# Optimization experiments

Measured on AMD Instinct MI355X. Metric: run time of the kernel, lower is better.

## Reference

```python
import jax, jax.numpy as jnp
import numpy as np

G = 4          # deformable groups (from offset_and_mask_dim = 3*4*3*3)
K = 9          # 3x3 kernel points
GN_GROUPS = 16 # GroupNorm groups as in DyHead


def conv2d(x, w, stride=1, pad=1, groups=1):
    return jax.lax.conv_general_dilated(
        x, w, (stride, stride), [(pad, pad), (pad, pad)],
        dimension_numbers=('NCHW', 'OIHW', 'NCHW'),
        feature_group_count=groups)


def dw_conv(x, w, scale, bias):
    # YOLO Conv with g=in_channels: depthwise 3x3 + folded BN + SiLU
    C = x.shape[1]
    y = conv2d(x, w, groups=C)
    y = y * scale[None, :, None, None] + bias[None, :, None, None]
    return y * jax.nn.sigmoid(y)


def offset_mask_conv(x, w, b):
    # Conv2d(C, 108, 3, padding=1, groups=4)
    return conv2d(x, w, groups=G) + b[None, :, None, None]


def split_offset_mask(om, use_softmax):
    # om: (N,108,H,W) -> offset (N,H,W,G,K,2) in pixels (dy,dx), mask (N,H,W,G,K)
    N, _, H, W = om.shape
    om = om.transpose(0, 2, 3, 1)
    offset = om[..., :2 * G * K].reshape(N, H, W, G, K, 2)
    m = om[..., 2 * G * K:].reshape(N, H, W, G, K)
    mask = jax.nn.softmax(m, axis=-1) if use_softmax else jax.nn.sigmoid(m)
    return offset, mask


def group_norm(x, gamma, beta, eps=1e-5):
    N, C, H, W = x.shape
    xg = x.reshape(N, GN_GROUPS, C // GN_GROUPS, H, W)
    mu = xg.mean((2, 3, 4), keepdims=True)
    var = xg.var((2, 3, 4), keepdims=True)
    xg = (xg - mu) * jax.lax.rsqrt(var + eps)
    return xg.reshape(N, C, H, W) * gamma[None, :, None, None] + beta[None, :, None, None]


def dcnv3_sample(x, offset, mask, stride):
    # DCNv3 core: group-wise deformable 3x3 bilinear sampling, zero padding.
    # x: (N,C,H,W); offset: (N,Ho,Wo,G,K,2); mask: (N,Ho,Wo,G,K) -> (N,C,Ho,Wo)
    N, C, H, W = x.shape
    Cg = C // G
    Ho, Wo = offset.shape[1], offset.shape[2]
    xg = x.transpose(0, 2, 3, 1).reshape(N, H, W, G, Cg)
    kk = jnp.arange(3, dtype=x.dtype) - 1.0
    ky = jnp.repeat(kk, 3)  # (9,)
    kx = jnp.tile(kk, 3)
    base_y = (jnp.arange(Ho, dtype=x.dtype) * stride)[None, :, None, None, None]
    base_x = (jnp.arange(Wo, dtype=x.dtype) * stride)[None, None, :, None, None]
    py = base_y + ky + offset[..., 0]   # (N,Ho,Wo,G,K)
    px = base_x + kx + offset[..., 1]
    y0 = jnp.floor(py)
    x0 = jnp.floor(px)
    wy = py - y0
    wx = px - x0
    y0i = y0.astype(jnp.int32)
    x0i = x0.astype(jnp.int32)
    n_idx = jnp.arange(N)[:, None, None, None, None]
    g_idx = jnp.arange(G)[None, None, None, :, None]
    acc = jnp.zeros((N, Ho, Wo, G, Cg), x.dtype)
    for dy in (0, 1):
        for dx in (0, 1):
            yi = y0i + dy
            xi = x0i + dx
            w = (wy if dy else 1.0 - wy) * (wx if dx else 1.0 - wx)
            valid = (yi >= 0) & (yi < H) & (xi >= 0) & (xi < W)
            w = w * valid.astype(x.dtype) * mask
            v = xg[n_idx, jnp.clip(yi, 0, H - 1), jnp.clip(xi, 0, W - 1), g_idx]  # (N,Ho,Wo,G,K,Cg)
            acc = acc + jnp.einsum('nhwgk,nhwgkc->nhwgc', w, v)
    return acc.reshape(N, Ho, Wo, C).transpose(0, 3, 1, 2)


def up_bilinear_ac(x, Ho, Wo):
    # bilinear, align_corners=True
    N, C, H, W = x.shape
    def coords(out, size):
        c = jnp.arange(out, dtype=jnp.float32) * ((size - 1) / max(out - 1, 1))
        i0 = jnp.floor(c).astype(jnp.int32)
        i1 = jnp.minimum(i0 + 1, size - 1)
        return i0, i1, (c - i0).astype(x.dtype)
    y0, y1, wy = coords(Ho, H)
    xc0, xc1, wx = coords(Wo, W)
    t = x[:, :, y0, :] * (1.0 - wy)[None, None, :, None] + x[:, :, y1, :] * wy[None, None, :, None]
    return t[:, :, :, xc0] * (1.0 - wx) + t[:, :, :, xc1] * wx


def scale_attn(f, w, b):
    # AdaptiveAvgPool2d(1) -> Conv 1x1 (C->1) -> ReLU -> HSigmoid(bias=3, divisor=6)
    y = f.mean((2, 3))                      # (N,C)
    a = jax.nn.relu(y @ w.T + b)            # (N,1)
    a = jnp.clip((a + 3.0) / 6.0, 0.0, 1.0)
    return f * a[:, :, None, None]


def dyrelu(f, w1, b1_, w2, b2_):
    # DyReLU with K2=True, use_bias=True, lambda_a=2, init_a=[1,0], init_b=[0,0]
    y = f.mean((2, 3))                      # (N,C)
    h = jax.nn.relu(y @ w1.T + b1_)
    z = jnp.clip(h @ w2.T + b2_ + 3.0, 0.0, 6.0) / 6.0  # h_sigmoid
    a1, b1, a2, b2 = jnp.split(z, 4, axis=1)
    a1 = (a1 - 0.5) * 2.0 + 1.0
    a2 = (a2 - 0.5) * 2.0
    b1 = b1 - 0.5
    b2 = b2 - 0.5
    bc = lambda t: t[:, :, None, None]
    return jnp.maximum(f * bc(a1) + bc(b1), f * bc(a2) + bc(b2))


def _forward(x0, x1, x2,
             dw_w_h, dw_s_h, dw_b_h, dw_w_m, dw_s_m, dw_b_m, dw_w_l, dw_s_l, dw_b_l,
             off_w, off_b,
             gn_g_h, gn_b_h, gn_g_m, gn_b_m, gn_g_l, gn_b_l,
             sa_w, sa_b, fc1_w, fc1_b, fc2_w, fc2_b):
    xs = [x0, x1, x2]
    outs = []
    for lvl in range(3):
        x = xs[lvl]
        mid_ = dw_conv(x, dw_w_m, dw_s_m, dw_b_m)
        off, msk = split_offset_mask(offset_mask_conv(mid_, off_w, off_b), use_softmax=False)
        mid_feat = group_norm(dcnv3_sample(x, off, msk, 1), gn_g_m, gn_b_m)
        sum_feat = scale_attn(mid_feat, sa_w, sa_b)
        n_lvls = 1
        if lvl > 0:
            xl = xs[lvl - 1]
            low_ = dw_conv(xl, dw_w_l, dw_s_l, dw_b_l)
            off, msk = split_offset_mask(offset_mask_conv(low_, off_w, off_b), use_softmax=True)
            off = off[:, ::2, ::2]   # stride-2 output grid
            msk = msk[:, ::2, ::2]
            low_feat = group_norm(dcnv3_sample(xl, off, msk, 2), gn_g_l, gn_b_l)
            sum_feat = sum_feat + scale_attn(low_feat, sa_w, sa_b)
            n_lvls += 1
        if lvl < 2:
            xh = xs[lvl + 1]
            high_ = dw_conv(xh, dw_w_h, dw_s_h, dw_b_h)
            off, msk = split_offset_mask(offset_mask_conv(high_, off_w, off_b), use_softmax=True)
            high_feat = group_norm(dcnv3_sample(xh, off, msk, 1), gn_g_h, gn_b_h)
            high_feat = up_bilinear_ac(high_feat, x.shape[2], x.shape[3])
            sum_feat = sum_feat + scale_attn(high_feat, sa_w, sa_b)
            n_lvls += 1
        outs.append(dyrelu(sum_feat / n_lvls, fc1_w, fc1_b, fc2_w, fc2_b))
    return tuple(outs)


def setup_inputs() -> dict:
    key = jax.random.key(0)
    ks = jax.random.split(key, 32)
    N, C = 4, 256
    f32 = jnp.float32
    nrm = lambda k, shape, s=1.0: jax.random.normal(k, shape, f32) * s
    inp = {
        'x0': nrm(ks[0], (N, C, 80, 80)),
        'x1': nrm(ks[1], (N, C, 40, 40)),
        'x2': nrm(ks[2], (N, C, 20, 20)),
        'dw_w_h': nrm(ks[3], (C, 1, 3, 3), 0.1),
        'dw_s_h': 1.0 + nrm(ks[4], (C,), 0.1),
        'dw_b_h': nrm(ks[5], (C,), 0.1),
        'dw_w_m': nrm(ks[6], (C, 1, 3, 3), 0.1),
        'dw_s_m': 1.0 + nrm(ks[7], (C,), 0.1),
        'dw_b_m': nrm(ks[8], (C,), 0.1),
        'dw_w_l': nrm(ks[9], (C, 1, 3, 3), 0.1),
        'dw_s_l': 1.0 + nrm(ks[10], (C,), 0.1),
        'dw_b_l': nrm(ks[11], (C,), 0.1),
        'off_w': nrm(ks[12], (108, C // G, 3, 3), 0.1),
        'off_b': nrm(ks[13], (108,), 0.1),
        'gn_g_h': 1.0 + nrm(ks[14], (C,), 0.1),
        'gn_b_h': nrm(ks[15], (C,), 0.1),
        'gn_g_m': 1.0 + nrm(ks[16], (C,), 0.1),
        'gn_b_m': nrm(ks[17], (C,), 0.1),
        'gn_g_l': 1.0 + nrm(ks[18], (C,), 0.1),
        'gn_b_l': nrm(ks[19], (C,), 0.1),
        'sa_w': nrm(ks[20], (1, C), 0.05),
        'sa_b': nrm(ks[21], (1,), 0.05),
        'fc1_w': nrm(ks[22], (C // 4, C), 0.05),
        'fc1_b': nrm(ks[23], (C // 4,), 0.05),
        'fc2_w': nrm(ks[24], (4 * C, C // 4), 0.05),
        'fc2_b': nrm(ks[25], (4 * C,), 0.1),
    }
    return inp


def reference(x0, x1, x2,
              dw_w_h, dw_s_h, dw_b_h, dw_w_m, dw_s_m, dw_b_m, dw_w_l, dw_s_l, dw_b_l,
              off_w, off_b,
              gn_g_h, gn_b_h, gn_g_m, gn_b_m, gn_g_l, gn_b_l,
              sa_w, sa_b, fc1_w, fc1_b, fc2_w, fc2_b):
    return _forward(x0, x1, x2,
                    dw_w_h, dw_s_h, dw_b_h, dw_w_m, dw_s_m, dw_b_m, dw_w_l, dw_s_l, dw_b_l,
                    off_w, off_b,
                    gn_g_h, gn_b_h, gn_g_m, gn_b_m, gn_g_l, gn_b_l,
                    sa_w, sa_b, fc1_w, fc1_b, fc2_w, fc2_b)
```

## Files before the change

kernel.cpp:

```cpp
#include <hip/hip_runtime.h>
#include <hip/hip_bf16.h>

#define C_ 256
#define G_ 4

typedef __attribute__((ext_vector_type(8))) short bf16x8;
typedef __attribute__((ext_vector_type(4))) float f32x4;

static __device__ __forceinline__ unsigned short f2bf(float x) {
    __hip_bfloat16 h = __float2bfloat16(x);
    return *(unsigned short*)&h;
}
static __device__ __forceinline__ float bf2f(unsigned short u) {
    return __uint_as_float((unsigned)u << 16);
}
static __device__ __forceinline__ float4 bf4(ushort4 u) {
    float4 r;
    r.x = bf2f(u.x);
    r.y = bf2f(u.y);
    r.z = bf2f(u.z);
    r.w = bf2f(u.w);
    return r;
}

// ... 33 lines not shown
__global__ __launch_bounds__(256) void k_transpose_b(TrP P) {
    __shared__ float tile[32][33];
    int b = blockIdx.x;
    int f = (b >= P.blk[1]) + (b >= P.blk[2]);
    int l = b - P.blk[f];
    int H = P.H[f], W = P.W[f], wtc = P.wtc[f];
    int nh = l / wtc, wtile = l - nh * wtc;
    int n = nh / H, h = nh % H;
    int w0 = wtile * 32, c0 = blockIdx.y * 32;
    const float* x = P.x[f];
    unsigned short* xtb = P.xtb[f];
    int tid = threadIdx.x;
    int i = tid / 32, j = tid % 32;
#pragma unroll
    for (int r = 0; r < 4; r++) {
        int c = c0 + i + r * 8;
        int w = w0 + j;
        tile[i + r * 8][j] = (w < W) ? x[((size_t)(n * C_ + c) * H + h) * W + w] : 0.f;
    }
    __syncthreads();
    int wj = tid >> 4, ci2 = (tid & 15) * 2;
#pragma unroll
    for (int r = 0; r < 2; r++) {
        int w = w0 + wj + r * 16;
        if (w < W) {
            ushort2 o;
            o.x = f2bf(tile[ci2][wj + r * 16]);
            o.y = f2bf(tile[ci2 + 1][wj + r * 16]);
            *(ushort2*)(xtb + ((size_t)(n * H + h) * W + w) * C_ + c0 + ci2) = o;
        }
    }
}

struct DwP {
    const unsigned short* xtb[7];
    unsigned short* out[7];
    const float* wdt[7];
    const float* sc[7];
    const float* bi[7];
    int H[7];
    int W[7];
    int blk[8];
};

__global__ __launch_bounds__(256) void k_dw_silu_b(DwP P) {
    int b = blockIdx.x;
    int f = (b >= P.blk[1]) + (b >= P.blk[2]) + (b >= P.blk[3]) + (b >= P.blk[4]) +
            (b >= P.blk[5]) + (b >= P.blk[6]);
    int H = P.H[f], W = P.W[f];
    const unsigned short* xtbf = P.xtb[f];
    unsigned short* outf = P.out[f];
    const float* wdt = P.wdt[f];
    int tid = threadIdx.x;
    int pw = tid >> 6, lane = tid & 63;
    int ch4 = lane << 2;
    int pix = (b - P.blk[f]) * 4 + pw;
    int w = pix % W, h = (pix / W) % H, n = pix / (W * H);
    const float4 s4 = *(const float4*)(P.sc[f] + ch4);
    const float4 b4 = *(const float4*)(P.bi[f] + ch4);
    const unsigned short* xb = xtbf + (size_t)n * H * W * C_ + ch4;
    float4 acc = {0.f, 0.f, 0.f, 0.f};
#pragma unroll
    for (int t = 0; t < 9; t++) {
        int hh = h + t / 3 - 1, ww = w + t % 3 - 1;
        if (hh >= 0 && hh < H && ww >= 0 && ww < W) {
            float4 wt = *(const float4*)(wdt + t * 256 + ch4);
            float4 xv = bf4(*(const ushort4*)(xb + (size_t)(hh * W + ww) * C_));
            acc.x += wt.x * xv.x;
            acc.y += wt.y * xv.y;
            acc.z += wt.z * xv.z;
            acc.w += wt.w * xv.w;
        }
    }
    float4 y;
    y.x = acc.x * s4.x + b4.x;
    y.y = acc.y * s4.y + b4.y;
    y.z = acc.z * s4.z + b4.z;
    y.w = acc.w * s4.w + b4.w;
    y.x = y.x / (1.f + __expf(-y.x));
    y.y = y.y / (1.f + __expf(-y.y));
    y.z = y.z / (1.f + __expf(-y.z));
    y.w = y.w / (1.f + __expf(-y.w));
    ushort4 o;
    o.x = f2bf(y.x);
    o.y = f2bf(y.y);
    o.z = f2bf(y.z);
    o.w = f2bf(y.w);
    *(ushort4*)(outf + (size_t)pix * C_ + ch4) = o;
}

struct OmP {
    const unsigned short* dwb[2];
    float* om[2];
};

template <int STRIDE, int TH, int TW>
__global__ __launch_bounds__(256) void k_offmask(OmP P, const unsigned short* __restrict__ wmf,
                                                 int Hs, int Ws, int Ho, int Wo) {
    constexpr int SR = STRIDE * (TH - 1) + 3;
    constexpr int SC = STRIDE * (TW - 1) + 3;
    constexpr int NV = SR * SC;
    constexpr int CP = 72;
    constexpr int TP = TH * TW;
    constexpr int NTILES = TP / 8;
    constexpr int PATCH_B = NV * CP * 2;
    constexpr int OMV_B = TP * 28 * 4;
    constexpr int LDS_B = PATCH_B > OMV_B ? PATCH_B : OMV_B;
    __shared__ __align__(16) char smem[LDS_B];
    unsigned short* patch = (unsigned short*)smem;
    float* omv = (float*)smem;

    int tid = threadIdx.x;
    int wv = tid >> 6, lane = tid & 63;
    int n16 = lane & 15, q = lane >> 4;
    int bx = blockIdx.x;
    int fi = bx >> 4;
    int n = (bx >> 2) & 3, g = bx & 3;
    const unsigned short* dwb = P.dwb[fi];
    float* om = P.om[fi];
    int ho0 = blockIdx.y * TH, wo0 = blockIdx.z * TW;
    int hs0 = ho0 * STRIDE - 1, ws0 = wo0 * STRIDE - 1;
    int HoWo = Ho * Wo;

    for (int idx = tid; idx < NV * 8; idx += 256) {
        int pp = idx >> 3;
        int c8 = (idx & 7) << 3;
        int hh = hs0 + pp / SC, ww = ws0 + pp % SC;
        uint4 v = {0u, 0u, 0u, 0u};
        if (hh >= 0 && hh < Hs && ww >= 0 && ww < Ws)
            v = *(const uint4*)(dwb + ((size_t)(n * Hs + hh) * Ws + ww) * C_ + g * 64 + c8);
        *(uint4*)(patch + pp * CP + c8) = v;
    }
    __syncthreads();

    int bchan = q << 3;
    const unsigned short* wg = wmf + (size_t)g * 32 * 576;

    if constexpr (NTILES >= 8) {
        int ntile = wv;
        int p = ntile * 16 + n16;
        int pr = p / TW, pc = p % TW;
        int pixbase = (pr * STRIDE) * SC + pc * STRIDE;
        f32x4 a0 = {0.f, 0.f, 0.f, 0.f}, a1 = {0.f, 0.f, 0.f, 0.f};
        for (int kk = 0; kk < 18; kk++) {
            int tap = kk >> 1;
            int ic0 = (kk & 1) << 5;
            int ppix = pixbase + (tap / 3) * SC + tap % 3;
            bf16x8 b = *(const bf16x8*)(patch + ppix * CP + ic0 + bchan);
            bf16x8 wa0 = *(const bf16x8*)(wg + (size_t)n16 * 576 + kk * 32 + bchan);
            bf16x8 wa1 = *(const bf16x8*)(wg + (size_t)(16 + n16) * 576 + kk * 32 + bchan);
            a0 = __builtin_amdgcn_mfma_f32_16x16x32_bf16(wa0, b, a0, 0, 0, 0);
            a1 = __builtin_amdgcn_mfma_f32_16x16x32_bf16(wa1, b, a1, 0, 0, 0);
        }
        __syncthreads();
#pragma unroll
        for (int r = 0; r < 4; r++) {
            int ol0 = q * 4 + r;
            omv[p * 28 + ol0] = a0[r];
            int ol1 = 16 + q * 4 + r;
            if (ol1 < 28) omv[p * 28 + ol1] = a1[r];
        }
    } else {
        int t = wv;
        bool active = t < NTILES;
        int ntile = t >> 1, mtile = t & 1;
        int p = ntile * 16 + n16;
        int pr = p / TW, pc = p % TW;
        int pixbase = (pr * STRIDE) * SC + pc * STRIDE;
        f32x4 acc = {0.f, 0.f, 0.f, 0.f};
        if (active) {
            for (int kk = 0; kk < 18; kk++) {
                int tap = kk >> 1;
                int ic0 = (kk & 1) << 5;
                int ppix = pixbase + (tap / 3) * SC + tap % 3;
                bf16x8 b = *(const bf16x8*)(patch + ppix * CP + ic0 + bchan);
                bf16x8 wa = *(const bf16x8*)(wg + (size_t)(mtile * 16 + n16) * 576 +
                                             kk * 32 + bchan);
                acc = __builtin_amdgcn_mfma_f32_16x16x32_bf16(wa, b, acc, 0, 0, 0);
            }
        }
        __syncthreads();
        if (active) {
#pragma unroll
            for (int r = 0; r < 4; r++) {
                int ol = mtile * 16 + q * 4 + r;
                if (ol < 28) omv[p * 28 + ol] = acc[r];
            }
        }
    }
    __syncthreads();

    float* omg = om + ((size_t)(g * 4 + n)) * HoWo * 28;
    for (int idx = tid; idx < TP * 7; idx += 256) {
        int p = idx / 7, c4 = idx % 7;
        int ho = ho0 + p / TW, wo = wo0 + p % TW;
        int pixn = ho * Wo + wo;
        *(float4*)(omg + (size_t)pixn * 28 + c4 * 4) = *(float4*)(omv + p * 28 + c4 * 4);
    }
}

struct SmP {
    const unsigned short* xtb[7];
    const float* om[7];
    float* raw[7];
    float* stats[7];
    int Hs[7];
    int Ws[7];
    int Wo[7];
    int HoWo[7];
    int stride[7];
    int softmax[7];
    int blk[8];
};

__global__ __launch_bounds__(256) void k_sample_b(SmP P, const float* __restrict__ bias) {
    int tid = threadIdx.x;
    int wv = tid >> 6, lane = tid & 63;
    int g = lane >> 4;
    int ch4 = lane << 2;
    int nb = gridDim.x;
    int per = nb >> 3, rem = nb & 7;
    int xcd = blockIdx.x & 7, bi = blockIdx.x >> 3;
    int logical = xcd * per + min(xcd, rem) + bi;
    int f = (logical >= P.blk[1]) + (logical >= P.blk[2]) + (logical >= P.blk[3]) +
            (logical >= P.blk[4]) + (logical >= P.blk[5]) + (logical >= P.blk[6]);
    const unsigned short* xtb = P.xtb[f];
    const float* om = P.om[f];
    float* raw = P.raw[f];
    float* stats = P.stats[f];
    int Hs = P.Hs[f], Ws = P.Ws[f], Wo = P.Wo[f], HoWo = P.HoWo[f];
    int stride = P.stride[f], softmax = P.softmax[f];
    int pix0 = (logical - P.blk[f]) * 8;
    int n = pix0 / HoWo;
    int pixn0 = pix0 - n * HoWo;

    __shared__ float lom[8 * 112];
    __shared__ float lb[108];
    __shared__ float sm[32][9];
    __shared__ float4 lw[288];
    __shared__ ushort4 li[288];
    __shared__ float lstat[32];

    if (tid < 224) {
        int gc = tid / 56, r2 = tid % 56;
        int pp = r2 / 7, c4 = r2 % 7;
        float4 v = *(const float4*)(om + ((size_t)(gc * 4 + n) * HoWo + pixn0 + pp) * 28 +
                                    c4 * 4);
        ((float4*)lom)[pp * 28 + gc * 7 + c4] = v;
    }
    if (tid < 108) lb[tid] = bias[tid];
    if (tid < 32) lstat[tid] = 0.f;
    __syncthreads();

    if (tid < 32) {
        int pp = tid >> 2, gs = tid & 3;
        float mv[9];
#pragma unroll
        for (int k = 0; k < 9; k++) {
            int ch = 72 + gs * 9 + k;
            int gc = ch / 27;
            mv[k] = lom[pp * 112 + gc * 28 + (ch - gc * 27)] + lb[ch];
        }
        if (softmax) {
            float mx = -1e30f;
#pragma unroll
            for (int k = 0; k < 9; k++) mx = fmaxf(mx, mv[k]);
            float ssum = 0.f;
#pragma unroll
            for (int k = 0; k < 9; k++) {
                mv[k] = __expf(mv[k] - mx);
                ssum += mv[k];
            }
            float inv = 1.f / ssum;
#pragma unroll
            for (int k = 0; k < 9; k++) sm[tid][k] = mv[k] * inv;
        } else {
#pragma unroll
            for (int k = 0; k < 9; k++) sm[tid][k] = 1.f / (1.f + __expf(-mv[k]));
        }
    }
    __syncthreads();

    for (int idx = tid; idx < 288; idx += 256) {
        int pg = idx / 9, k = idx % 9;
        int pp = pg >> 2, gs = pg & 3;
        int chy = gs * 18 + 2 * k, chx = chy + 1;
        int gcy = chy / 27, gcx = chx / 27;
        float oy = lom[pp * 112 + gcy * 28 + (chy - gcy * 27)] + lb[chy];
        float ox = lom[pp * 112 + gcx * 28 + (chx - gcx * 27)] + lb[chx];
        int pixn = pixn0 + pp;
        int ho = pixn / Wo, wo = pixn % Wo;
        float py = (float)(ho * stride + k / 3 - 1) + oy;
        float px = (float)(wo * stride + k % 3 - 1) + ox;
        float y0f = floorf(py), x0f = floorf(px);
        int y0 = (int)y0f, x0 = (int)x0f;
        float wy = py - y0f, wx = px - x0f;
        int y1 = y0 + 1, x1 = x0 + 1;
        float v0y = (y0 >= 0 && y0 < Hs) ? 1.f : 0.f;
        float v1y = (y1 >= 0 && y1 < Hs) ? 1.f : 0.f;
        float v0x = (x0 >= 0 && x0 < Ws) ? 1.f : 0.f;
        float v1x = (x1 >= 0 && x1 < Ws) ? 1.f : 0.f;
        int y0c = min(max(y0, 0), Hs - 1), y1c = min(max(y1, 0), Hs - 1);
        int x0c = min(max(x0, 0), Ws - 1), x1c = min(max(x1, 0), Ws - 1);
        float m_ = sm[pg][k];
        float4 w4;
        w4.x = (1.f - wy) * (1.f - wx) * v0y * v0x * m_;
        w4.y = (1.f - wy) * wx * v0y * v1x * m_;
        w4.z = wy * (1.f - wx) * v1y * v0x * m_;
        w4.w = wy * wx * v1y * v1x * m_;
        ushort4 i4;
        i4.x = (unsigned short)(y0c * Ws + x0c);
        i4.y = (unsigned short)(y0c * Ws + x1c);
        i4.z = (unsigned short)(y1c * Ws + x0c);
        i4.w = (unsigned short)(y1c * Ws + x1c);
        lw[pp * 36 + gs * 9 + k] = w4;
        li[pp * 36 + gs * 9 + k] = i4;
    }
    __syncthreads();

    int pA = wv * 2, pB = wv * 2 + 1;
    const unsigned short* xb = xtb + (size_t)n * Hs * Ws * C_ + ch4;
    float4 aA = {0.f, 0.f, 0.f, 0.f}, aB = {0.f, 0.f, 0.f, 0.f};
#pragma unroll
    for (int k = 0; k < 9; k++) {
        float4 wA = lw[pA * 36 + g * 9 + k];
        ushort4 iA = li[pA * 36 + g * 9 + k];
        float4 wB = lw[pB * 36 + g * 9 + k];
        ushort4 iB = li[pB * 36 + g * 9 + k];
        float4 vA0 = bf4(*(const ushort4*)(xb + ((size_t)iA.x << 8)));
        float4 vA1 = bf4(*(const ushort4*)(xb + ((size_t)iA.y << 8)));
        float4 vA2 = bf4(*(const ushort4*)(xb + ((size_t)iA.z << 8)));
        float4 vA3 = bf4(*(const ushort4*)(xb + ((size_t)iA.w << 8)));
        float4 vB0 = bf4(*(const ushort4*)(xb + ((size_t)iB.x << 8)));
        float4 vB1 = bf4(*(const ushort4*)(xb + ((size_t)iB.y << 8)));
        float4 vB2 = bf4(*(const ushort4*)(xb + ((size_t)iB.z << 8)));
        float4 vB3 = bf4(*(const ushort4*)(xb + ((size_t)iB.w << 8)));
        aA.x += wA.x * vA0.x + wA.y * vA1.x + wA.z * vA2.x + wA.w * vA3.x;
        aA.y += wA.x * vA0.y + wA.y * vA1.y + wA.z * vA2.y + wA.w * vA3.y;
        aA.z += wA.x * vA0.z + wA.y * vA1.z + wA.z * vA2.z + wA.w * vA3.z;
        aA.w += wA.x * vA0.w + wA.y * vA1.w + wA.z * vA2.w + wA.w * vA3.w;
        aB.x += wB.x * vB0.x + wB.y * vB1.x + wB.z * vB2.x + wB.w * vB3.x;
        aB.y += wB.x * vB0.y + wB.y * vB1.y + wB.z * vB2.y + wB.w * vB3.y;
        aB.z += wB.x * vB0.z + wB.y * vB1.z + wB.z * vB2.z + wB.w * vB3.z;
        aB.w += wB.x * vB0.w + wB.y * vB1.w + wB.z * vB2.w + wB.w * vB3.w;
    }
    *(float4*)(raw + (size_t)(pix0 + pA) * C_ + ch4) = aA;
    *(float4*)(raw + (size_t)(pix0 + pB) * C_ + ch4) = aB;
    float gs = aA.x + aA.y + aA.z + aA.w + aB.x + aB.y + aB.z + aB.w;
    float gss = aA.x * aA.x + aA.y * aA.y + aA.z * aA.z + aA.w * aA.w + aB.x * aB.x +
                aB.y * aB.y + aB.z * aB.z + aB.w * aB.w;
#pragma unroll
    for (int o = 2; o; o >>= 1) {
        gs += __shfl_down(gs, o, 4);
        gss += __shfl_down(gss, o, 4);
    }
    if ((lane & 3) == 0) {
        atomicAdd(&lstat[(lane >> 2) * 2 + 0], gs);
        atomicAdd(&lstat[(lane >> 2) * 2 + 1], gss);
    }
    __syncthreads();
    if (tid < 32) atomicAdd(&stats[n * 32 + tid], lstat[tid]);
}

struct GnP {
    const float* raw[5];
    float* fin[5];
    const float* stats[5];
    float* cmean[5];
    const float* gamma[5];
    const float* beta[5];
    int Hr[5];
    int Wr[5];
    int Hf[5];
    int Wf[5];
    int blk[6];
};

__global__ __launch_bounds__(256) void k_gnup_b(GnP P) {
    int b = blockIdx.x;
    int f = (b >= P.blk[1]) + (b >= P.blk[2]) + (b >= P.blk[3]) + (b >= P.blk[4]);
    int Hr = P.Hr[f], Wr = P.Wr[f], Hf = P.Hf[f], Wf = P.Wf[f];
    const float* raw = P.raw[f];
    float* fin = P.fin[f];
    const float* stats = P.stats[f];
    float* cmean = P.cmean[f];
    int HWf = Hf * Wf;
    int spn = (HWf + 63) >> 6;
    int lb_ = b - P.blk[f];
    int n = lb_ / spn;
    int p0 = (lb_ % spn) << 6;
    int tid = threadIdx.x;
    int wv = tid >> 6, lane = tid & 63;
    int ch4 = lane << 2;
    int gg = lane >> 2;
    float cnt = 16.f * Hr * Wr;
    float s1 = stats[(n * 16 + gg) * 2], s2 = stats[(n * 16 + gg) * 2 + 1];
    float mu = s1 / cnt;
    float var = s2 / cnt - mu * mu;
    float rs = rsqrtf(var + 1e-5f);
    float4 g4 = *(const float4*)(P.gamma[f] + ch4);
    float4 b4 = *(const float4*)(P.beta[f] + ch4);
    float4 ga, be;
    ga.x = g4.x * rs; be.x = b4.x - mu * ga.x;
    ga.y = g4.y * rs; be.y = b4.y - mu * ga.y;
    ga.z = g4.z * rs; be.z = b4.z - mu * ga.z;
    ga.w = g4.w * rs; be.w = b4.w - mu * ga.w;
    bool up = (Hf != Hr);
    float sys = up ? (float)((double)(Hr - 1) / (double)(Hf - 1)) : 0.f;
    float sxs = up ? (float)((double)(Wr - 1) / (double)(Wf - 1)) : 0.f;
    float4 csum = {0.f, 0.f, 0.f, 0.f};
    __shared__ float cs[4][256];
// ... 267 lines not shown
    float* RAW_l0mid = SH;
    float* RAW_l0high = FINC;
    float* RAW_l1mid = FINB;
    float* RAW_l1low = FINB + 1638400;
    float* RAW_l1high = FINB + 3276800;
    float* RAW_l2mid = FINB + 3686400;
    float* RAW_l2low = FINB + 4096000;
    float* FIN_l0mid = FINA;
    float* FIN_l0high = FINB;
    float* FIN_l1mid = XTBF;
    float* FIN_l1low = XTBF + 1638400;
    float* FIN_l1high = SH;
    float* FIN_l2mid = XTBF + 3276800;
    float* FIN_l2low = XTBF + 3686400;
    float* COEF = FINC;
    float* AF = FINC + 12288;

    k_prep<<<(4 * 32 * 576 + 6912 + 8064 + 255) / 256, 256, 0, stream>>>(
        off_w, dw_w_h, dw_w_m, dw_w_l, WMFB, DWT, STATS);

    {
        TrP tp{};
        tp.x[0] = x0; tp.xtb[0] = XTB0; tp.H[0] = 80; tp.W[0] = 80; tp.wtc[0] = 3;
        tp.x[1] = x1; tp.xtb[1] = XTB1; tp.H[1] = 40; tp.W[1] = 40; tp.wtc[1] = 2;
        tp.x[2] = x2; tp.xtb[2] = XTB2; tp.H[2] = 20; tp.W[2] = 20; tp.wtc[2] = 1;
        tp.blk[0] = 0; tp.blk[1] = 960; tp.blk[2] = 1280; tp.blk[3] = 1360;
        k_transpose_b<<<dim3(1360, 8), 256, 0, stream>>>(tp);
    }

    unsigned short* DWB_x0mid = SHB;
    unsigned short* DWB_x0low = SHB + 6553600;
    unsigned short* DWB_x1high = FINAB;
    unsigned short* DWB_x1mid = FINAB + 1638400;
    unsigned short* DWB_x1low = FINAB + 3276800;
    unsigned short* DWB_x2high = FINAB + 4915200;
    unsigned short* DWB_x2mid = FINAB + 5324800;

    {
        DwP dp{};
        dp.xtb[0] = XTB0; dp.out[0] = DWB_x0mid;  dp.wdt[0] = DWT + 1 * 2304;
        dp.sc[0] = dw_s_m; dp.bi[0] = dw_b_m; dp.H[0] = 80; dp.W[0] = 80;
        dp.xtb[1] = XTB0; dp.out[1] = DWB_x0low;  dp.wdt[1] = DWT + 2 * 2304;
        dp.sc[1] = dw_s_l; dp.bi[1] = dw_b_l; dp.H[1] = 80; dp.W[1] = 80;
        dp.xtb[2] = XTB1; dp.out[2] = DWB_x1high; dp.wdt[2] = DWT + 0 * 2304;
        dp.sc[2] = dw_s_h; dp.bi[2] = dw_b_h; dp.H[2] = 40; dp.W[2] = 40;
        dp.xtb[3] = XTB1; dp.out[3] = DWB_x1mid;  dp.wdt[3] = DWT + 1 * 2304;
        dp.sc[3] = dw_s_m; dp.bi[3] = dw_b_m; dp.H[3] = 40; dp.W[3] = 40;
        dp.xtb[4] = XTB1; dp.out[4] = DWB_x1low;  dp.wdt[4] = DWT + 2 * 2304;
        dp.sc[4] = dw_s_l; dp.bi[4] = dw_b_l; dp.H[4] = 40; dp.W[4] = 40;
        dp.xtb[5] = XTB2; dp.out[5] = DWB_x2high; dp.wdt[5] = DWT + 0 * 2304;
        dp.sc[5] = dw_s_h; dp.bi[5] = dw_b_h; dp.H[5] = 20; dp.W[5] = 20;
        dp.xtb[6] = XTB2; dp.out[6] = DWB_x2mid;  dp.wdt[6] = DWT + 1 * 2304;
        dp.sc[6] = dw_s_m; dp.bi[6] = dw_b_m; dp.H[6] = 20; dp.W[6] = 20;
        dp.blk[0] = 0;     dp.blk[1] = 6400;  dp.blk[2] = 12800; dp.blk[3] = 14400;
        dp.blk[4] = 16000; dp.blk[5] = 17600; dp.blk[6] = 18000; dp.blk[7] = 18400;
        k_dw_silu_b<<<18400, 256, 0, stream>>>(dp);
    }

    {
        OmP p1{{DWB_x0mid, DWB_x0mid}, {OM_l0mid, OM_l0mid}};
        k_offmask<1, 8, 8><<<dim3(16, 10, 10), 256, 0, stream>>>(p1, WMFB, 80, 80, 80, 80);
        OmP p2{{DWB_x1high, DWB_x1mid}, {OM_l0high, OM_l1mid}};
        k_offmask<1, 4, 8><<<dim3(32, 10, 5), 256, 0, stream>>>(p2, WMFB, 40, 40, 40, 40);
        OmP p3{{DWB_x0low, DWB_x0low}, {OM_l1low, OM_l1low}};
        k_offmask<2, 4, 8><<<dim3(16, 10, 5), 256, 0, stream>>>(p3, WMFB, 80, 80, 40, 40);
        OmP p4{{DWB_x2high, DWB_x2mid}, {OM_l1high, OM_l2mid}};
        k_offmask<1, 4, 4><<<dim3(32, 5, 5), 256, 0, stream>>>(p4, WMFB, 20, 20, 20, 20);
        OmP p5{{DWB_x1low, DWB_x1low}, {OM_l2low, OM_l2low}};
        k_offmask<2, 4, 4><<<dim3(16, 5, 5), 256, 0, stream>>>(p5, WMFB, 40, 40, 20, 20);
    }

    {
        SmP sp{};
        sp.xtb[0] = XTB0; sp.om[0] = OM_l0mid;  sp.raw[0] = RAW_l0mid;  sp.stats[0] = STATS + 0 * 128;
        sp.Hs[0] = 80; sp.Ws[0] = 80; sp.Wo[0] = 80; sp.HoWo[0] = 6400; sp.stride[0] = 1; sp.softmax[0] = 0;
        sp.xtb[1] = XTB1; sp.om[1] = OM_l0high; sp.raw[1] = RAW_l0high; sp.stats[1] = STATS + 1 * 128;
        sp.Hs[1] = 40; sp.Ws[1] = 40; sp.Wo[1] = 40; sp.HoWo[1] = 1600; sp.stride[1] = 1; sp.softmax[1] = 1;
        sp.xtb[2] = XTB1; sp.om[2] = OM_l1mid;  sp.raw[2] = RAW_l1mid;  sp.stats[2] = STATS + 2 * 128;
        sp.Hs[2] = 40; sp.Ws[2] = 40; sp.Wo[2] = 40; sp.HoWo[2] = 1600; sp.stride[2] = 1; sp.softmax[2] = 0;
        sp.xtb[3] = XTB0; sp.om[3] = OM_l1low;  sp.raw[3] = RAW_l1low;  sp.stats[3] = STATS + 3 * 128;
        sp.Hs[3] = 80; sp.Ws[3] = 80; sp.Wo[3] = 40; sp.HoWo[3] = 1600; sp.stride[3] = 2; sp.softmax[3] = 1;
        sp.xtb[4] = XTB2; sp.om[4] = OM_l1high; sp.raw[4] = RAW_l1high; sp.stats[4] = STATS + 4 * 128;
        sp.Hs[4] = 20; sp.Ws[4] = 20; sp.Wo[4] = 20; sp.HoWo[4] = 400;  sp.stride[4] = 1; sp.softmax[4] = 1;
        sp.xtb[5] = XTB2; sp.om[5] = OM_l2mid;  sp.raw[5] = RAW_l2mid;  sp.stats[5] = STATS + 5 * 128;
        sp.Hs[5] = 20; sp.Ws[5] = 20; sp.Wo[5] = 20; sp.HoWo[5] = 400;  sp.stride[5] = 1; sp.softmax[5] = 0;
        sp.xtb[6] = XTB1; sp.om[6] = OM_l2low;  sp.raw[6] = RAW_l2low;  sp.stats[6] = STATS + 6 * 128;
        sp.Hs[6] = 40; sp.Ws[6] = 40; sp.Wo[6] = 20; sp.HoWo[6] = 400;  sp.stride[6] = 2; sp.softmax[6] = 1;
        sp.blk[0] = 0;    sp.blk[1] = 3200; sp.blk[2] = 4000; sp.blk[3] = 4800;
        sp.blk[4] = 5600; sp.blk[5] = 5800; sp.blk[6] = 6000; sp.blk[7] = 6200;
        k_sample_b<<<6200, 256, 0, stream>>>(sp, off_b);
    }

    {
        GnP gp{};
        gp.raw[0] = RAW_l0mid; gp.fin[0] = FIN_l0mid; gp.stats[0] = STATS + 0 * 128;
        gp.cmean[0] = CMEAN + 0 * 1024; gp.gamma[0] = gn_g_m; gp.beta[0] = gn_b_m;
        gp.Hr[0] = 80; gp.Wr[0] = 80; gp.Hf[0] = 80; gp.Wf[0] = 80;
        gp.blk[0] = 0; gp.blk[1] = 400; gp.blk[2] = 400;
        gp.blk[3] = 400; gp.blk[4] = 400; gp.blk[5] = 400;
        k_gnup_b<<<400, 256, 0, stream>>>(gp);
    }
    {
        GnP gp{};
        gp.raw[0] = RAW_l1mid;  gp.fin[0] = FIN_l1mid;  gp.stats[0] = STATS + 2 * 128;
        gp.cmean[0] = CMEAN + 2 * 1024; gp.gamma[0] = gn_g_m; gp.beta[0] = gn_b_m;
        gp.Hr[0] = 40; gp.Wr[0] = 40; gp.Hf[0] = 40; gp.Wf[0] = 40;
        gp.raw[1] = RAW_l1low;  gp.fin[1] = FIN_l1low;  gp.stats[1] = STATS + 3 * 128;
        gp.cmean[1] = CMEAN + 3 * 1024; gp.gamma[1] = gn_g_l; gp.beta[1] = gn_b_l;
        gp.Hr[1] = 40; gp.Wr[1] = 40; gp.Hf[1] = 40; gp.Wf[1] = 40;
        gp.raw[2] = RAW_l1high; gp.fin[2] = FIN_l1high; gp.stats[2] = STATS + 4 * 128;
        gp.cmean[2] = CMEAN + 4 * 1024; gp.gamma[2] = gn_g_h; gp.beta[2] = gn_b_h;
        gp.Hr[2] = 20; gp.Wr[2] = 20; gp.Hf[2] = 40; gp.Wf[2] = 40;
        gp.raw[3] = RAW_l2mid;  gp.fin[3] = FIN_l2mid;  gp.stats[3] = STATS + 5 * 128;
        gp.cmean[3] = CMEAN + 5 * 1024; gp.gamma[3] = gn_g_m; gp.beta[3] = gn_b_m;
        gp.Hr[3] = 20; gp.Wr[3] = 20; gp.Hf[3] = 20; gp.Wf[3] = 20;
        gp.raw[4] = RAW_l2low;  gp.fin[4] = FIN_l2low;  gp.stats[4] = STATS + 6 * 128;
        gp.cmean[4] = CMEAN + 6 * 1024; gp.gamma[4] = gn_g_l; gp.beta[4] = gn_b_l;
        gp.Hr[4] = 20; gp.Wr[4] = 20; gp.Hf[4] = 20; gp.Wf[4] = 20;
        gp.blk[0] = 0; gp.blk[1] = 100; gp.blk[2] = 200;
        gp.blk[3] = 300; gp.blk[4] = 328; gp.blk[5] = 356;
        k_gnup_b<<<356, 256, 0, stream>>>(gp);
    }
// ... 32 lines not shown
```

Before: 428.5 us.

## Merge offset-mask launches into one batched kernel and widen per-lane channel vectors

The five templated offset/mask conv launches become a single kernel that picks its feature map from a block-range table. Tile geometry now comes from runtime shift and reciprocal parameters instead of template constants. The depthwise conv kernel and the deformable sampling kernel now have each lane handle 8 bf16 channels with 16-byte loads, so a block covers twice as many pixels (the depthwise grid is halved). The intent is to cut launch overhead, tail effects between small launches, and the number of memory transactions. The cost is losing compile-time specialization in the offset/mask kernel and higher register use per lane.

```diff
diff --git a/kernel.cpp b/kernel.cpp
--- a/kernel.cpp
+++ b/kernel.cpp
@@ -109,105 +109,126 @@
     unsigned short* outf = P.out[f];
     const float* wdt = P.wdt[f];
     int tid = threadIdx.x;
-    int pw = tid >> 6, lane = tid & 63;
-    int ch4 = lane << 2;
-    int pix = (b - P.blk[f]) * 4 + pw;
+    int wv = tid >> 6, lane = tid & 63;
+    int half = lane >> 5, l5 = lane & 31;
+    int ch8 = l5 << 3;
+    int pix = (b - P.blk[f]) * 8 + wv * 2 + half;
     int w = pix % W, h = (pix / W) % H, n = pix / (W * H);
-    const float4 s4 = *(const float4*)(P.sc[f] + ch4);
-    const float4 b4 = *(const float4*)(P.bi[f] + ch4);
-    const unsigned short* xb = xtbf + (size_t)n * H * W * C_ + ch4;
-    float4 acc = {0.f, 0.f, 0.f, 0.f};
+    const float4 sA = *(const float4*)(P.sc[f] + ch8);
+    const float4 sB = *(const float4*)(P.sc[f] + ch8 + 4);
+    const float4 bA = *(const float4*)(P.bi[f] + ch8);
+    const float4 bB = *(const float4*)(P.bi[f] + ch8 + 4);
+    const unsigned short* xb = xtbf + (size_t)n * H * W * C_ + ch8;
+    float4 accA = {0.f, 0.f, 0.f, 0.f}, accB = {0.f, 0.f, 0.f, 0.f};
 #pragma unroll
     for (int t = 0; t < 9; t++) {
         int hh = h + t / 3 - 1, ww = w + t % 3 - 1;
         if (hh >= 0 && hh < H && ww >= 0 && ww < W) {
-            float4 wt = *(const float4*)(wdt + t * 256 + ch4);
-            float4 xv = bf4(*(const ushort4*)(xb + (size_t)(hh * W + ww) * C_));
-            acc.x += wt.x * xv.x;
-            acc.y += wt.y * xv.y;
-            acc.z += wt.z * xv.z;
-            acc.w += wt.w * xv.w;
-        }
-    }
-    float4 y;
-    y.x = acc.x * s4.x + b4.x;
-    y.y = acc.y * s4.y + b4.y;
-    y.z = acc.z * s4.z + b4.z;
-    y.w = acc.w * s4.w + b4.w;
-    y.x = y.x / (1.f + __expf(-y.x));
-    y.y = y.y / (1.f + __expf(-y.y));
-    y.z = y.z / (1.f + __expf(-y.z));
-    y.w = y.w / (1.f + __expf(-y.w));
-    ushort4 o;
-    o.x = f2bf(y.x);
-    o.y = f2bf(y.y);
-    o.z = f2bf(y.z);
-    o.w = f2bf(y.w);
-    *(ushort4*)(outf + (size_t)pix * C_ + ch4) = o;
-}
-
-struct OmP {
-    const unsigned short* dwb[2];
-    float* om[2];
+            bf16x8 xv = *(const bf16x8*)(xb + (size_t)(hh * W + ww) * C_);
+            float4 wa = *(const float4*)(wdt + t * 256 + ch8);
+            float4 wb = *(const float4*)(wdt + t * 256 + ch8 + 4);
+            accA.x += wa.x * bf2f((unsigned short)xv[0]);
+            accA.y += wa.y * bf2f((unsigned short)xv[1]);
+            accA.z += wa.z * bf2f((unsigned short)xv[2]);
+            accA.w += wa.w * bf2f((unsigned short)xv[3]);
+            accB.x += wb.x * bf2f((unsigned short)xv[4]);
+            accB.y += wb.y * bf2f((unsigned short)xv[5]);
+            accB.z += wb.z * bf2f((unsigned short)xv[6]);
+            accB.w += wb.w * bf2f((unsigned short)xv[7]);
+        }
+    }
+    float y0 = accA.x * sA.x + bA.x, y1 = accA.y * sA.y + bA.y;
+    float y2 = accA.z * sA.z + bA.z, y3 = accA.w * sA.w + bA.w;
+    float y4 = accB.x * sB.x + bB.x, y5 = accB.y * sB.y + bB.y;
+    float y6 = accB.z * sB.z + bB.z, y7 = accB.w * sB.w + bB.w;
+    y0 = y0 / (1.f + __expf(-y0));
+    y1 = y1 / (1.f + __expf(-y1));
+    y2 = y2 / (1.f + __expf(-y2));
+    y3 = y3 / (1.f + __expf(-y3));
+    y4 = y4 / (1.f + __expf(-y4));
+    y5 = y5 / (1.f + __expf(-y5));
+    y6 = y6 / (1.f + __expf(-y6));
+    y7 = y7 / (1.f + __expf(-y7));
+    uint4 ov;
+    ov.x = (unsigned)f2bf(y0) | ((unsigned)f2bf(y1) << 16);
+    ov.y = (unsigned)f2bf(y2) | ((unsigned)f2bf(y3) << 16);
+    ov.z = (unsigned)f2bf(y4) | ((unsigned)f2bf(y5) << 16);
+    ov.w = (unsigned)f2bf(y6) | ((unsigned)f2bf(y7) << 16);
+    *(uint4*)(outf + (size_t)pix * C_ + ch8) = ov;
+}
+
+struct OmP7 {
+    const unsigned short* dwb[7];
+    float* om[7];
+    int Hs[7], Ws[7], Wo[7], HoWo[7];
+    int ss[7];
+    int ths[7], tws[7];
+    int SR[7], SC[7], Msc[7];
+    int nz[7], Mnz[7];
+    int blk[8];
 };
 
-template <int STRIDE, int TH, int TW>
-__global__ __launch_bounds__(256) void k_offmask(OmP P, const unsigned short* __restrict__ wmf,
-                                                 int Hs, int Ws, int Ho, int Wo) {
-    constexpr int SR = STRIDE * (TH - 1) + 3;
-    constexpr int SC = STRIDE * (TW - 1) + 3;
-    constexpr int NV = SR * SC;
-    constexpr int CP = 72;
-    constexpr int TP = TH * TW;
-    constexpr int NTILES = TP / 8;
-    constexpr int PATCH_B = NV * CP * 2;
-    constexpr int OMV_B = TP * 28 * 4;
-    constexpr int LDS_B = PATCH_B > OMV_B ? PATCH_B : OMV_B;
-    __shared__ __align__(16) char smem[LDS_B];
+__global__ __launch_bounds__(256) void k_offmask_b(OmP7 P,
+                                                   const unsigned short* __restrict__ wmf) {
+    __shared__ __align__(16) char smem[22032];
     unsigned short* patch = (unsigned short*)smem;
     float* omv = (float*)smem;
 
     int tid = threadIdx.x;
     int wv = tid >> 6, lane = tid & 63;
     int n16 = lane & 15, q = lane >> 4;
-    int bx = blockIdx.x;
-    int fi = bx >> 4;
-    int n = (bx >> 2) & 3, g = bx & 3;
-    const unsigned short* dwb = P.dwb[fi];
-    float* om = P.om[fi];
-    int ho0 = blockIdx.y * TH, wo0 = blockIdx.z * TW;
-    int hs0 = ho0 * STRIDE - 1, ws0 = wo0 * STRIDE - 1;
-    int HoWo = Ho * Wo;
+    int b = blockIdx.x;
+    int f = (b >= P.blk[1]) + (b >= P.blk[2]) + (b >= P.blk[3]) + (b >= P.blk[4]) +
+            (b >= P.blk[5]) + (b >= P.blk[6]);
+    int l = b - P.blk[f];
+    int n = (l >> 2) & 3, g = l & 3;
+    int tile = l >> 4;
+    int nz = P.nz[f];
+    int ty = (tile * P.Mnz[f]) >> 16;
+    int tz = tile - ty * nz;
+    int ss = P.ss[f], ths = P.ths[f], tws = P.tws[f];
+    int TW = 1 << tws;
+    int SR = P.SR[f], SC = P.SC[f], Msc = P.Msc[f];
+    int NV = SR * SC;
+    int Hs = P.Hs[f], Ws = P.Ws[f], Wo = P.Wo[f], HoWo = P.HoWo[f];
+    int ho0 = ty << ths, wo0 = tz << tws;
+    int hs0 = (ho0 << ss) - 1, ws0 = (wo0 << ss) - 1;
+    const unsigned short* dwb = P.dwb[f];
+    float* om = P.om[f];
 
     for (int idx = tid; idx < NV * 8; idx += 256) {
         int pp = idx >> 3;
         int c8 = (idx & 7) << 3;
-        int hh = hs0 + pp / SC, ww = ws0 + pp % SC;
+        int pq = (pp * Msc) >> 16;
+        int hh = hs0 + pq, ww = ws0 + (pp - pq * SC);
         uint4 v = {0u, 0u, 0u, 0u};
         if (hh >= 0 && hh < Hs && ww >= 0 && ww < Ws)
             v = *(const uint4*)(dwb + ((size_t)(n * Hs + hh) * Ws + ww) * C_ + g * 64 + c8);
-        *(uint4*)(patch + pp * CP + c8) = v;
+        *(uint4*)(patch + pp * 72 + c8) = v;
     }
     __syncthreads();
 
     int bchan = q << 3;
     const unsigned short* wg = wmf + (size_t)g * 32 * 576;
-
-    if constexpr (NTILES >= 8) {
-        int ntile = wv;
-        int p = ntile * 16 + n16;
-        int pr = p / TW, pc = p % TW;
-        int pixbase = (pr * STRIDE) * SC + pc * STRIDE;
+    int TP = 1 << (ths + tws);
+    int sc1 = SC, sc2 = SC * 2;
+
+    if (TP == 64) {
+        int p = wv * 16 + n16;
+        int pr = p >> tws, pc = p & (TW - 1);
+        int pixbase = (pr << ss) * SC + (pc << ss);
         f32x4 a0 = {0.f, 0.f, 0.f, 0.f}, a1 = {0.f, 0.f, 0.f, 0.f};
+#pragma unroll
         for (int kk = 0; kk < 18; kk++) {
             int tap = kk >> 1;
             int ic0 = (kk & 1) << 5;
-            int ppix = pixbase + (tap / 3) * SC + tap % 3;
-            bf16x8 b = *(const bf16x8*)(patch + ppix * CP + ic0 + bchan);
+            int tr = tap / 3, tc = tap % 3;
+            int ppix = pixbase + (tr == 0 ? 0 : (tr == 1 ? sc1 : sc2)) + tc;
+            bf16x8 bb = *(const bf16x8*)(patch + ppix * 72 + ic0 + bchan);
             bf16x8 wa0 = *(const bf16x8*)(wg + (size_t)n16 * 576 + kk * 32 + bchan);
             bf16x8 wa1 = *(const bf16x8*)(wg + (size_t)(16 + n16) * 576 + kk * 32 + bchan);
-            a0 = __builtin_amdgcn_mfma_f32_16x16x32_bf16(wa0, b, a0, 0, 0, 0);
-            a1 = __builtin_amdgcn_mfma_f32_16x16x32_bf16(wa1, b, a1, 0, 0, 0);
+            a0 = __builtin_amdgcn_mfma_f32_16x16x32_bf16(wa0, bb, a0, 0, 0, 0);
+            a1 = __builtin_amdgcn_mfma_f32_16x16x32_bf16(wa1, bb, a1, 0, 0, 0);
         }
         __syncthreads();
 #pragma unroll
@@ -218,22 +239,25 @@
             if (ol1 < 28) omv[p * 28 + ol1] = a1[r];
         }
     } else {
+        int NT = TP >> 3;
         int t = wv;
-        bool active = t < NTILES;
+        bool active = t < NT;
         int ntile = t >> 1, mtile = t & 1;
         int p = ntile * 16 + n16;
-        int pr = p / TW, pc = p % TW;
-        int pixbase = (pr * STRIDE) * SC + pc * STRIDE;
+        int pr = p >> tws, pc = p & (TW - 1);
+        int pixbase = (pr << ss) * SC + (pc << ss);
         f32x4 acc = {0.f, 0.f, 0.f, 0.f};
         if (active) {
+#pragma unroll
             for (int kk = 0; kk < 18; kk++) {
                 int tap = kk >> 1;
                 int ic0 = (kk & 1) << 5;
-                int ppix = pixbase + (tap / 3) * SC + tap % 3;
-                bf16x8 b = *(const bf16x8*)(patch + ppix * CP + ic0 + bchan);
+                int tr = tap / 3, tc = tap % 3;
+                int ppix = pixbase + (tr == 0 ? 0 : (tr == 1 ? sc1 : sc2)) + tc;
+                bf16x8 bb = *(const bf16x8*)(patch + ppix * 72 + ic0 + bchan);
                 bf16x8 wa = *(const bf16x8*)(wg + (size_t)(mtile * 16 + n16) * 576 +
                                              kk * 32 + bchan);
-                acc = __builtin_amdgcn_mfma_f32_16x16x32_bf16(wa, b, acc, 0, 0, 0);
+                acc = __builtin_amdgcn_mfma_f32_16x16x32_bf16(wa, bb, acc, 0, 0, 0);
             }
         }
         __syncthreads();
@@ -249,8 +273,9 @@
 
     float* omg = om + ((size_t)(g * 4 + n)) * HoWo * 28;
     for (int idx = tid; idx < TP * 7; idx += 256) {
-        int p = idx / 7, c4 = idx % 7;
-        int ho = ho0 + p / TW, wo = wo0 + p % TW;
+        int p = (idx * 9363) >> 16;
+        int c4 = idx - p * 7;
+        int ho = ho0 + (p >> tws), wo = wo0 + (p & (TW - 1));
         int pixn = ho * Wo + wo;
         *(float4*)(omg + (size_t)pixn * 28 + c4 * 4) = *(float4*)(omv + p * 28 + c4 * 4);
     }
@@ -273,8 +298,9 @@
 __global__ __launch_bounds__(256) void k_sample_b(SmP P, const float* __restrict__ bias) {
     int tid = threadIdx.x;
     int wv = tid >> 6, lane = tid & 63;
-    int g = lane >> 4;
-    int ch4 = lane << 2;
+    int halfp = lane >> 5, l5 = lane & 31;
+    int g = l5 >> 3;
+    int ch8 = l5 << 3;
     int nb = gridDim.x;
     int per = nb >> 3, rem = nb & 7;
     int xcd = blockIdx.x & 7, bi = blockIdx.x >> 3;
@@ -375,45 +401,44 @@
     }
     __syncthreads();
 
-    int pA = wv * 2, pB = wv * 2 + 1;
-    const unsigned short* xb = xtb + (size_t)n * Hs * Ws * C_ + ch4;
-    float4 aA = {0.f, 0.f, 0.f, 0.f}, aB = {0.f, 0.f, 0.f, 0.f};
+    int px = wv * 2 + halfp;
+    const unsigned short* xb = xtb + (size_t)n * Hs * Ws * C_ + ch8;
+    float4 aL = {0.f, 0.f, 0.f, 0.f}, aH = {0.f, 0.f, 0.f, 0.f};
 #pragma unroll
     for (int k = 0; k < 9; k++) {
-        float4 wA = lw[pA * 36 + g * 9 + k];
-        ushort4 iA = li[pA * 36 + g * 9 + k];
-        float4 wB = lw[pB * 36 + g * 9 + k];
-        ushort4 iB = li[pB * 36 + g * 9 + k];
-        float4 vA0 = bf4(*(const ushort4*)(xb + ((size_t)iA.x << 8)));
-        float4 vA1 = bf4(*(const ushort4*)(xb + ((size_t)iA.y << 8)));
-        float4 vA2 = bf4(*(const ushort4*)(xb + ((size_t)iA.z << 8)));
-        float4 vA3 = bf4(*(const ushort4*)(xb + ((size_t)iA.w << 8)));
-        float4 vB0 = bf4(*(const ushort4*)(xb + ((size_t)iB.x << 8)));
-        float4 vB1 = bf4(*(const ushort4*)(xb + ((size_t)iB.y << 8)));
-        float4 vB2 = bf4(*(const ushort4*)(xb + ((size_t)iB.z << 8)));
-        float4 vB3 = bf4(*(const ushort4*)(xb + ((size_t)iB.w << 8)));
-        aA.x += wA.x * vA0.x + wA.y * vA1.x + wA.z * vA2.x + wA.w * vA3.x;
-        aA.y += wA.x * vA0.y + wA.y * vA1.y + wA.z * vA2.y + wA.w * vA3.y;
-        aA.z += wA.x * vA0.z + wA.y * vA1.z + wA.z * vA2.z + wA.w * vA3.z;
-        aA.w += wA.x * vA0.w + wA.y * vA1.w + wA.z * vA2.w + wA.w * vA3.w;
-        aB.x += wB.x * vB0.x + wB.y * vB1.x + wB.z * vB2.x + wB.w * vB3.x;
-        aB.y += wB.x * vB0.y + wB.y * vB1.y + wB.z * vB2.y + wB.w * vB3.y;
-        aB.z += wB.x * vB0.z + wB.y * vB1.z + wB.z * vB2.z + wB.w * vB3.z;
-        aB.w += wB.x * vB0.w + wB.y * vB1.w + wB.z * vB2.w + wB.w * vB3.w;
-    }
-    *(float4*)(raw + (size_t)(pix0 + pA) * C_ + ch4) = aA;
-    *(float4*)(raw + (size_t)(pix0 + pB) * C_ + ch4) = aB;
-    float gs = aA.x + aA.y + aA.z + aA.w + aB.x + aB.y + aB.z + aB.w;
-    float gss = aA.x * aA.x + aA.y * aA.y + aA.z * aA.z + aA.w * aA.w + aB.x * aB.x +
-                aB.y * aB.y + aB.z * aB.z + aB.w * aB.w;
-#pragma unroll
-    for (int o = 2; o; o >>= 1) {
-        gs += __shfl_down(gs, o, 4);
-        gss += __shfl_down(gss, o, 4);
-    }
-    if ((lane & 3) == 0) {
-        atomicAdd(&lstat[(lane >> 2) * 2 + 0], gs);
-        atomicAdd(&lstat[(lane >> 2) * 2 + 1], gss);
+        float4 w4 = lw[px * 36 + g * 9 + k];
+        ushort4 i4 = li[px * 36 + g * 9 + k];
+        bf16x8 v0 = *(const bf16x8*)(xb + ((size_t)i4.x << 8));
+        bf16x8 v1 = *(const bf16x8*)(xb + ((size_t)i4.y << 8));
+        bf16x8 v2 = *(const bf16x8*)(xb + ((size_t)i4.z << 8));
+        bf16x8 v3 = *(const bf16x8*)(xb + ((size_t)i4.w << 8));
+        aL.x += w4.x * bf2f((unsigned short)v0[0]) + w4.y * bf2f((unsigned short)v1[0]) +
+                w4.z * bf2f((unsigned short)v2[0]) + w4.w * bf2f((unsigned short)v3[0]);
+        aL.y += w4.x * bf2f((unsigned short)v0[1]) + w4.y * bf2f((unsigned short)v1[1]) +
+                w4.z * bf2f((unsigned short)v2[1]) + w4.w * bf2f((unsigned short)v3[1]);
+        aL.z += w4.x * bf2f((unsigned short)v0[2]) + w4.y * bf2f((unsigned short)v1[2]) +
+                w4.z * bf2f((unsigned short)v2[2]) + w4.w * bf2f((unsigned short)v3[2]);
+        aL.w += w4.x * bf2f((unsigned short)v0[3]) + w4.y * bf2f((unsigned short)v1[3]) +
+                w4.z * bf2f((unsigned short)v2[3]) + w4.w * bf2f((unsigned short)v3[3]);
+        aH.x += w4.x * bf2f((unsigned short)v0[4]) + w4.y * bf2f((unsigned short)v1[4]) +
+                w4.z * bf2f((unsigned short)v2[4]) + w4.w * bf2f((unsigned short)v3[4]);
+        aH.y += w4.x * bf2f((unsigned short)v0[5]) + w4.y * bf2f((unsigned short)v1[5]) +
+                w4.z * bf2f((unsigned short)v2[5]) + w4.w * bf2f((unsigned short)v3[5]);
+        aH.z += w4.x * bf2f((unsigned short)v0[6]) + w4.y * bf2f((unsigned short)v1[6]) +
+                w4.z * bf2f((unsigned short)v2[6]) + w4.w * bf2f((unsigned short)v3[6]);
+        aH.w += w4.x * bf2f((unsigned short)v0[7]) + w4.y * bf2f((unsigned short)v1[7]) +
+                w4.z * bf2f((unsigned short)v2[7]) + w4.w * bf2f((unsigned short)v3[7]);
+    }
+    *(float4*)(raw + (size_t)(pix0 + px) * C_ + ch8) = aL;
+    *(float4*)(raw + (size_t)(pix0 + px) * C_ + ch8 + 4) = aH;
+    float gs = aL.x + aL.y + aL.z + aL.w + aH.x + aH.y + aH.z + aH.w;
+    float gss = aL.x * aL.x + aL.y * aL.y + aL.z * aL.z + aL.w * aL.w + aH.x * aH.x +
+                aH.y * aH.y + aH.z * aH.z + aH.w * aH.w;
+    gs += __shfl_down(gs, 1, 2);
+    gss += __shfl_down(gss, 1, 2);
+    if ((lane & 1) == 0) {
+        atomicAdd(&lstat[(l5 >> 1) * 2 + 0], gs);
+        atomicAdd(&lstat[(l5 >> 1) * 2 + 1], gss);
     }
     __syncthreads();
     if (tid < 32) atomicAdd(&stats[n * 32 + tid], lstat[tid]);
@@ -787,22 +812,32 @@
         dp.sc[5] = dw_s_h; dp.bi[5] = dw_b_h; dp.H[5] = 20; dp.W[5] = 20;
         dp.xtb[6] = XTB2; dp.out[6] = DWB_x2mid;  dp.wdt[6] = DWT + 1 * 2304;
         dp.sc[6] = dw_s_m; dp.bi[6] = dw_b_m; dp.H[6] = 20; dp.W[6] = 20;
-        dp.blk[0] = 0;     dp.blk[1] = 6400;  dp.blk[2] = 12800; dp.blk[3] = 14400;
-        dp.blk[4] = 16000; dp.blk[5] = 17600; dp.blk[6] = 18000; dp.blk[7] = 18400;
-        k_dw_silu_b<<<18400, 256, 0, stream>>>(dp);
+        dp.blk[0] = 0;    dp.blk[1] = 3200; dp.blk[2] = 6400; dp.blk[3] = 7200;
+        dp.blk[4] = 8000; dp.blk[5] = 8800; dp.blk[6] = 9000; dp.blk[7] = 9200;
+        k_dw_silu_b<<<9200, 256, 0, stream>>>(dp);
     }
 
     {
-        OmP p1{{DWB_x0mid, DWB_x0mid}, {OM_l0mid, OM_l0mid}};
-        k_offmask<1, 8, 8><<<dim3(16, 10, 10), 256, 0, stream>>>(p1, WMFB, 80, 80, 80, 80);
-        OmP p2{{DWB_x1high, DWB_x1mid}, {OM_l0high, OM_l1mid}};
-        k_offmask<1, 4, 8><<<dim3(32, 10, 5), 256, 0, stream>>>(p2, WMFB, 40, 40, 40, 40);
-        OmP p3{{DWB_x0low, DWB_x0low}, {OM_l1low, OM_l1low}};
-        k_offmask<2, 4, 8><<<dim3(16, 10, 5), 256, 0, stream>>>(p3, WMFB, 80, 80, 40, 40);
-        OmP p4{{DWB_x2high, DWB_x2mid}, {OM_l1high, OM_l2mid}};
-        k_offmask<1, 4, 4><<<dim3(32, 5, 5), 256, 0, stream>>>(p4, WMFB, 20, 20, 20, 20);
-        OmP p5{{DWB_x1low, DWB_x1low}, {OM_l2low, OM_l2low}};
-        k_offmask<2, 4, 4><<<dim3(16, 5, 5), 256, 0, stream>>>(p5, WMFB, 40, 40, 20, 20);
+        OmP7 op{};
+        auto setf = [&](int i, const unsigned short* dwb, float* om, int Hs, int Ws,
+                        int Wo, int HoWo, int ss, int ths, int tws, int SR, int SC,
+                        int nz) {
+            op.dwb[i] = dwb; op.om[i] = om;
+            op.Hs[i] = Hs; op.Ws[i] = Ws; op.Wo[i] = Wo; op.HoWo[i] = HoWo;
+            op.ss[i] = ss; op.ths[i] = ths; op.tws[i] = tws;
+            op.SR[i] = SR; op.SC[i] = SC; op.Msc[i] = (65536 + SC - 1) / SC;
+            op.nz[i] = nz; op.Mnz[i] = (65536 + nz - 1) / nz;
+        };
+        setf(0, DWB_x0mid,  OM_l0mid,  80, 80, 80, 6400, 0, 3, 3, 10, 10, 10);
+        setf(1, DWB_x1high, OM_l0high, 40, 40, 40, 1600, 0, 2, 3, 6,  10, 5);
+        setf(2, DWB_x1mid,  OM_l1mid,  40, 40, 40, 1600, 0, 2, 3, 6,  10, 5);
+        setf(3, DWB_x0low,  OM_l1low,  80, 80, 40, 1600, 1, 2, 3, 9,  17, 5);
+        setf(4, DWB_x2high, OM_l1high, 20, 20, 20, 400,  0, 2, 2, 6,  6,  5);
+        setf(5, DWB_x2mid,  OM_l2mid,  20, 20, 20, 400,  0, 2, 2, 6,  6,  5);
+        setf(6, DWB_x1low,  OM_l2low,  40, 40, 20, 400,  1, 2, 2, 9,  9,  5);
+        op.blk[0] = 0;    op.blk[1] = 1600; op.blk[2] = 2400; op.blk[3] = 3200;
+        op.blk[4] = 4000; op.blk[5] = 4400; op.blk[6] = 4800; op.blk[7] = 5200;
+        k_offmask_b<<<5200, 256, 0, stream>>>(op, WMFB);
     }
 
     {
```

Result: faster. 405.6 us (-5.4%).
